# Kernel tuning notes

Measured on AMD Instinct MI355X. Metric: run time of the kernel, lower is better.

Reference implementation:

```python
import jax, jax.numpy as jnp
import numpy as np

N_NODES = 100000
N_EDGES = 1600000
F_IN = 128
N_GRAPHS = 1000
NUM_CLASSES = 2


def setup_inputs() -> dict:
    key = jax.random.key(0)
    ks = jax.random.split(key, 12)
    x = jax.random.normal(ks[0], (N_NODES, F_IN), jnp.float32)
    edge_index = jax.random.randint(ks[1], (2, N_EDGES), 0, N_NODES, dtype=jnp.int32)
    edge_weight = jnp.ones((N_EDGES,), jnp.float32)
    node_graph_index = jnp.sort(
        jax.random.randint(ks[2], (N_NODES,), 0, N_GRAPHS, dtype=jnp.int32))
    s = 0.05
    params = {
        'W0': jax.random.normal(ks[3], (F_IN, 64), jnp.float32) * s,
        'b0': jnp.zeros((64,), jnp.float32),
        'W1': jax.random.normal(ks[4], (64, 32), jnp.float32) * s,
        'b1': jnp.zeros((32,), jnp.float32),
        'Wm1': jax.random.normal(ks[5], (32, 128), jnp.float32) * s,
        'bm1': jnp.zeros((128,), jnp.float32),
        'Wm2': jax.random.normal(ks[6], (128, NUM_CLASSES), jnp.float32) * s,
        'bm2': jnp.zeros((NUM_CLASSES,), jnp.float32),
    }
    return dict(x=x, edge_index=edge_index, edge_weight=edge_weight,
                node_graph_index=node_graph_index, **params)


def _gcn_norm(edge_index, edge_weight, n_nodes):
    # renormalization trick: add self-loops, D^-1/2 (A+I) D^-1/2
    loop = jnp.arange(n_nodes, dtype=edge_index.dtype)
    src = jnp.concatenate([edge_index[0], loop])
    dst = jnp.concatenate([edge_index[1], loop])
    w = jnp.concatenate([edge_weight, jnp.ones((n_nodes,), edge_weight.dtype)])
    deg = jax.ops.segment_sum(w, dst, num_segments=n_nodes)
    dinv = jnp.where(deg > 0, jax.lax.rsqrt(jnp.maximum(deg, 1e-12)), 0.0)
    norm_w = dinv[src] * w * dinv[dst]
    return src, dst, norm_w


def _gcn_layer(h, src, dst, norm_w, W, b, n_nodes):
    m = h @ W                                # [N, out] dense transform first
    msg = m[src] * norm_w[:, None]           # [E+N, out] irregular gather
    agg = jax.ops.segment_sum(msg, dst, num_segments=n_nodes)
    return jax.nn.relu(agg + b)


def reference(x, edge_index, edge_weight, node_graph_index,
              W0, b0, W1, b1, Wm1, bm1, Wm2, bm2):
    n_nodes = x.shape[0]
    src, dst, norm_w = _gcn_norm(edge_index, edge_weight, n_nodes)
    h = _gcn_layer(x, src, dst, norm_w, W0, b0, n_nodes)   # GCN 64 + relu
    # dropout is identity at inference (training=False default)
    h = _gcn_layer(h, src, dst, norm_w, W1, b1, n_nodes)   # GCN 32 + relu
    g = jax.ops.segment_sum(h, node_graph_index, num_segments=N_GRAPHS)  # sum_pool
    g = jax.nn.relu(g @ Wm1 + bm1)
    logits = g @ Wm2 + bm2
    return logits
```

## Files before the change

### kernel.cpp

```cpp
#include <hip/hip_runtime.h>
#include <hip/hip_bf16.h>

#define F_IN 128
#define NPB 256
#define NPB_SH 8
#define MAXB 512
#define CHUNK 4096
#define CAP 5120

typedef __attribute__((ext_vector_type(8))) short short8;
typedef __attribute__((ext_vector_type(4))) float f32x4;


__device__ __forceinline__ float bf2f(unsigned short u) {
    return __uint_as_float(((unsigned int)u) << 16);
}
__device__ __forceinline__ unsigned short f2bf(float f) {
    unsigned int x = __float_as_uint(f);
    x += 0x7FFFu + ((x >> 16) & 1u);
    return (unsigned short)(x >> 16);
}
__device__ __forceinline__ void bf8_fma(float w, uint4 r, float* a) {
    a[0] = fmaf(w, __uint_as_float(r.x << 16), a[0]);
    a[1] = fmaf(w, __uint_as_float(r.x & 0xFFFF0000u), a[1]);
    a[2] = fmaf(w, __uint_as_float(r.y << 16), a[2]);
    a[3] = fmaf(w, __uint_as_float(r.y & 0xFFFF0000u), a[3]);
    a[4] = fmaf(w, __uint_as_float(r.z << 16), a[4]);
    a[5] = fmaf(w, __uint_as_float(r.z & 0xFFFF0000u), a[5]);
    a[6] = fmaf(w, __uint_as_float(r.w << 16), a[6]);
    a[7] = fmaf(w, __uint_as_float(r.w & 0xFFFF0000u), a[7]);
}

__global__ __launch_bounds__(256) void prep_w_kernel(
    const float* __restrict__ W0, const float* __restrict__ W1,
    unsigned short* __restrict__ W0t, unsigned short* __restrict__ W1t,
    int* __restrict__ gcursor, float* __restrict__ Gbuf,
    int nbucket, int gtot) {
    int t = blockIdx.x * 256 + threadIdx.x;
    int stride = gridDim.x * 256;
    for (int o = t; o < 64 * 128; o += stride) {
        int n = o >> 7, k = o & 127;
        W0t[o] = f2bf(W0[k * 64 + n]);
    }
    for (int o = t; o < 32 * 64; o += stride) {
        int n = o >> 6, k = o & 63;
        W1t[o] = f2bf(W1[k * 32 + n]);
    }
    for (int o = t; o < nbucket; o += stride) gcursor[o] = 0;
    for (int o = t; o < gtot; o += stride) Gbuf[o] = 0.f;
}

__global__ __launch_bounds__(1024) void bucket_fused_kernel(
    const int* __restrict__ src, const int* __restrict__ dst,
    const float* __restrict__ ew, int* __restrict__ gcursor,
    int2* __restrict__ tmp, int E, int nbucket) {
    __shared__ int hist[MAXB];
    __shared__ int gbase[MAXB];
    const int tid = threadIdx.x;
    const int e0 = blockIdx.x * CHUNK;
    const int e1 = min(e0 + CHUNK, E);
    for (int b = tid; b < nbucket; b += 1024) hist[b] = 0;
    __syncthreads();
    const int e = e0 + (tid << 2);
    const bool vec = (e + 4 <= e1);
    const int nsc = vec ? 0 : max(0, e1 - e);
    int4 d4 = make_int4(0, 0, 0, 0);
    if (vec) {
        d4 = *(const int4*)(dst + e);
        atomicAdd(&hist[d4.x >> NPB_SH], 1);
        atomicAdd(&hist[d4.y >> NPB_SH], 1);
        atomicAdd(&hist[d4.z >> NPB_SH], 1);
        atomicAdd(&hist[d4.w >> NPB_SH], 1);
    } else {
        for (int j = 0; j < nsc; ++j) {
            int d = dst[e + j];
            ((int*)&d4)[j] = d;
            atomicAdd(&hist[d >> NPB_SH], 1);
        }
    }
    __syncthreads();
    for (int b = tid; b < nbucket; b += 1024) {
        int h = hist[b];
        gbase[b] = (h > 0) ? atomicAdd(&gcursor[b], h) : 0;
        hist[b] = 0;
    }
    __syncthreads();
    if (vec) {
        int4 s4 = *(const int4*)(src + e);
        float4 w4 = *(const float4*)(ew + e);
        {
            int d = d4.x, b = d >> NPB_SH;
            int r = atomicAdd(&hist[b], 1);
            tmp[(size_t)b * CAP + gbase[b] + r] =
                make_int2(s4.x | ((d & (NPB - 1)) << 17), __float_as_int(w4.x));
        }
        {
            int d = d4.y, b = d >> NPB_SH;
            int r = atomicAdd(&hist[b], 1);
            tmp[(size_t)b * CAP + gbase[b] + r] =
                make_int2(s4.y | ((d & (NPB - 1)) << 17), __float_as_int(w4.y));
        }
        {
            int d = d4.z, b = d >> NPB_SH;
            int r = atomicAdd(&hist[b], 1);
            tmp[(size_t)b * CAP + gbase[b] + r] =
                make_int2(s4.z | ((d & (NPB - 1)) << 17), __float_as_int(w4.z));
        }
        {
            int d = d4.w, b = d >> NPB_SH;
            int r = atomicAdd(&hist[b], 1);
            tmp[(size_t)b * CAP + gbase[b] + r] =
                make_int2(s4.w | ((d & (NPB - 1)) << 17), __float_as_int(w4.w));
        }
    } else {
        for (int j = 0; j < nsc; ++j) {
            int d = ((int*)&d4)[j];
            int b = d >> NPB_SH;
            int r = atomicAdd(&hist[b], 1);
            tmp[(size_t)b * CAP + gbase[b] + r] =
                make_int2(src[e + j] | ((d & (NPB - 1)) << 17), __float_as_int(ew[e + j]));
        }
    }
}

__global__ __launch_bounds__(1024) void csr_kernel(
    const int2* __restrict__ tmp, const int* __restrict__ gcursor,
    int2* __restrict__ es, int* __restrict__ rstart, int* __restrict__ rend,
    float* __restrict__ dinv, int N) {
    __shared__ int cnt[256];
    __shared__ float dw[256];
    __shared__ int off[256];
    __shared__ int cur[256];
    const int t = threadIdx.x;
    const int n0 = blockIdx.x << NPB_SH;
    const size_t seg = (size_t)blockIdx.x * CAP;
    if (t < 256) {
        cnt[t] = 0;
        dw[t] = 0.f;
    }
    __syncthreads();
    const int count = gcursor[blockIdx.x];
    const int pairs = count >> 1;
    for (int i = t; i < pairs; i += 1024) {
        int4 v = *(const int4*)(tmp + seg + 2 * i);
        int d0 = v.x >> 17, d1 = v.z >> 17;
        atomicAdd(&cnt[d0], 1);
        atomicAdd(&dw[d0], __int_as_float(v.y));
        atomicAdd(&cnt[d1], 1);
        atomicAdd(&dw[d1], __int_as_float(v.w));
    }
    if ((count & 1) && t == 0) {
        int2 e2 = tmp[seg + count - 1];
        int d = e2.x >> 17;
        atomicAdd(&cnt[d], 1);
        atomicAdd(&dw[d], __int_as_float(e2.y));
    }
    __syncthreads();
    if (t < 256) off[t] = cnt[t];
    __syncthreads();
    for (int o = 1; o < 256; o <<= 1) {
        int x = 0;
        if (t >= o && t < 256) x = off[t - o];
        __syncthreads();
        if (t < 256) off[t] += x;
        __syncthreads();
    }
    if (t < 256) {
        int v = cnt[t];
        int excl = off[t] - v;
        cur[t] = excl;
        int n = n0 + t;
        if (n < N) {
            rstart[n] = (int)seg + excl;
            rend[n] = (int)seg + excl + v;
            dinv[n] = rsqrtf(fmaxf(1.f + dw[t], 1e-12f));
        }
    }
    __syncthreads();
    for (int i = t; i < pairs; i += 1024) {
        int4 v = *(const int4*)(tmp + seg + 2 * i);
        int d0 = v.x >> 17, d1 = v.z >> 17;
        int r0 = atomicAdd(&cur[d0], 1);
        es[seg + r0] = make_int2(v.x & 0x1FFFF, v.y);
        int r1 = atomicAdd(&cur[d1], 1);
        es[seg + r1] = make_int2(v.z & 0x1FFFF, v.w);
    }
    if ((count & 1) && t == 0) {
        int2 e2 = tmp[seg + count - 1];
        int d = e2.x >> 17;
        int r = atomicAdd(&cur[d], 1);
        es[seg + r] = make_int2(e2.x & 0x1FFFF, e2.y);
    }
}

__global__ __launch_bounds__(256) void gemm1_mfma_kernel(
    const float* __restrict__ X, const unsigned short* __restrict__ W0t,
    const float* __restrict__ dinv, unsigned short* __restrict__ M, int N) {
    __shared__ unsigned short Bs[64][136];
    const int tid = threadIdx.x;
    for (int i = tid; i < 64 * 32; i += 256) {
        int n = i >> 5, k4 = i & 31;
        ushort4 v = ((const ushort4*)W0t)[i];
        *(ushort4*)&Bs[n][k4 * 4] = v;
    }
    __syncthreads();
    const int wave = tid >> 6, lane = tid & 63;
    const int m = lane & 15, q = lane >> 4;
    const int rowA = blockIdx.x * 64 + wave * 16 + m;
    const bool rok = rowA < N;
    const float* xrow = X + (size_t)rowA * 128;
    f32x4 acc[4] = {};
#pragma unroll
    for (int ks = 0; ks < 4; ++ks) {
        int k0 = ks * 32 + q * 8;
        float4 u0 = make_float4(0.f, 0.f, 0.f, 0.f);
        float4 u1 = make_float4(0.f, 0.f, 0.f, 0.f);
        if (rok) {
            u0 = *(const float4*)(xrow + k0);
            u1 = *(const float4*)(xrow + k0 + 4);
        }
        short8 a;
        a[0] = (short)f2bf(u0.x); a[1] = (short)f2bf(u0.y);
        a[2] = (short)f2bf(u0.z); a[3] = (short)f2bf(u0.w);
        a[4] = (short)f2bf(u1.x); a[5] = (short)f2bf(u1.y);
        a[6] = (short)f2bf(u1.z); a[7] = (short)f2bf(u1.w);
#pragma unroll
        for (int ct = 0; ct < 4; ++ct) {
            short8 b = *(const short8*)&Bs[ct * 16 + m][k0];
            acc[ct] = __builtin_amdgcn_mfma_f32_16x16x32_bf16(a, b, acc[ct], 0, 0, 0);
        }
    }
#pragma unroll
    for (int r = 0; r < 4; ++r) {
        int crow = blockIdx.x * 64 + wave * 16 + q * 4 + r;
        if (crow < N) {
            float d = dinv[crow];
#pragma unroll
            for (int ct = 0; ct < 4; ++ct)
                M[(size_t)crow * 64 + ct * 16 + m] = f2bf(acc[ct][r] * d);
        }
    }
}

__global__ __launch_bounds__(256) void gemm2_mfma_kernel(
    const unsigned short* __restrict__ H1, const unsigned short* __restrict__ W1t,
    const float* __restrict__ dinv, unsigned short* __restrict__ M, int N) {
    __shared__ unsigned short Bs[32][72];
    const int tid = threadIdx.x;
    for (int i = tid; i < 32 * 16; i += 256) {
        int n = i >> 4, k4 = i & 15;
        ushort4 v = ((const ushort4*)W1t)[i];
        *(ushort4*)&Bs[n][k4 * 4] = v;
    }
    __syncthreads();
    const int wave = tid >> 6, lane = tid & 63;
    const int m = lane & 15, q = lane >> 4;
    const int rowA = blockIdx.x * 64 + wave * 16 + m;
    const bool rok = rowA < N;
    const short8 az = {0, 0, 0, 0, 0, 0, 0, 0};
    f32x4 acc[2] = {};
#pragma unroll
    for (int ks = 0; ks < 2; ++ks) {
        int k0 = ks * 32 + q * 8;
        short8 a = rok ? *(const short8*)(H1 + (size_t)rowA * 64 + k0) : az;
#pragma unroll
        for (int ct = 0; ct < 2; ++ct) {
            short8 b = *(const short8*)&Bs[ct * 16 + m][k0];
            acc[ct] = __builtin_amdgcn_mfma_f32_16x16x32_bf16(a, b, acc[ct], 0, 0, 0);
        }
    }
#pragma unroll
    for (int r = 0; r < 4; ++r) {
        int crow = blockIdx.x * 64 + wave * 16 + q * 4 + r;
        if (crow < N) {
            float d = dinv[crow];
#pragma unroll
            for (int ct = 0; ct < 2; ++ct)
                M[(size_t)crow * 32 + ct * 16 + m] = f2bf(acc[ct][r] * d);
        }
    }
}

__global__ __launch_bounds__(256) void pull1_kernel(
    const int* __restrict__ rstart, const int* __restrict__ rend,
    const int2* __restrict__ es, const unsigned short* __restrict__ M,
    const float* __restrict__ dinv, const float* __restrict__ bias,
    unsigned short* __restrict__ H1, int N) {
    const int lane = threadIdx.x & 63;
    const int wave = threadIdx.x >> 6;
    const int nd = lane >> 5;
    const int node = blockIdx.x * 8 + wave * 2 + nd;
    if (node >= N) return;
    const int c = lane & 7;
    const int q = (lane >> 3) & 3;
    float acc[8] = {0.f, 0.f, 0.f, 0.f, 0.f, 0.f, 0.f, 0.f};
    if (q == 0) {
        uint4 r = *(const uint4*)(M + (size_t)node * 64 + c * 8);
        bf8_fma(1.f, r, acc);
    }
    const int b = rstart[node], e = rend[node];
    const int len = e - b;
    const int base = len >> 2, rem = len & 3;
    int p = b + q * base + min(q, rem);
    const int pe = p + base + (q < rem ? 1 : 0);
    for (; p + 2 <= pe; p += 2) {
        int4 v = *(const int4*)(es + p);
        uint4 r0 = *(const uint4*)(M + (size_t)v.x * 64 + c * 8);
        uint4 r1 = *(const uint4*)(M + (size_t)v.z * 64 + c * 8);
        bf8_fma(__int_as_float(v.y), r0, acc);
        bf8_fma(__int_as_float(v.w), r1, acc);
    }
    if (p < pe) {
        int2 ed = es[p];
        uint4 r = *(const uint4*)(M + (size_t)ed.x * 64 + c * 8);
        bf8_fma(__int_as_float(ed.y), r, acc);
    }
#pragma unroll
    for (int off = 8; off <= 16; off <<= 1)
#pragma unroll
        for (int k = 0; k < 8; ++k) acc[k] += __shfl_xor(acc[k], off);
    if (q == 0) {
        float d = dinv[node];
        const float* bp = bias + c * 8;
        float4 b0v = *(const float4*)(bp);
        float4 b1v = *(const float4*)(bp + 4);
        unsigned short o[8];
        o[0] = f2bf(fmaxf(fmaf(d, acc[0], b0v.x), 0.f));
        o[1] = f2bf(fmaxf(fmaf(d, acc[1], b0v.y), 0.f));
        o[2] = f2bf(fmaxf(fmaf(d, acc[2], b0v.z), 0.f));
        o[3] = f2bf(fmaxf(fmaf(d, acc[3], b0v.w), 0.f));
        o[4] = f2bf(fmaxf(fmaf(d, acc[4], b1v.x), 0.f));
        o[5] = f2bf(fmaxf(fmaf(d, acc[5], b1v.y), 0.f));
        o[6] = f2bf(fmaxf(fmaf(d, acc[6], b1v.z), 0.f));
        o[7] = f2bf(fmaxf(fmaf(d, acc[7], b1v.w), 0.f));
        uint4 pk;
        pk.x = (unsigned int)o[0] | ((unsigned int)o[1] << 16);
        pk.y = (unsigned int)o[2] | ((unsigned int)o[3] << 16);
        pk.z = (unsigned int)o[4] | ((unsigned int)o[5] << 16);
        pk.w = (unsigned int)o[6] | ((unsigned int)o[7] << 16);
        *(uint4*)(H1 + (size_t)node * 64 + c * 8) = pk;
    }
}

__global__ __launch_bounds__(256) void pull2_pool_kernel(
    const int* __restrict__ rstart, const int* __restrict__ rend,
    const int2* __restrict__ es, const unsigned short* __restrict__ M,
    const float* __restrict__ dinv, const float* __restrict__ bias,
    const int* __restrict__ ngi, float* __restrict__ g, int N) {
    __shared__ float4 sh[16][8];
    __shared__ int sgx[16];
    const int t = threadIdx.x;
    const int lane = t & 63;
    const int nl = t >> 4;
    const int node = blockIdx.x * 16 + nl;
    const int c = lane & 3;
    const int q = (lane >> 2) & 3;
    const bool valid = node < N;
    float acc[8] = {0.f, 0.f, 0.f, 0.f, 0.f, 0.f, 0.f, 0.f};
    if (valid) {
        if (q == 0) {
            uint4 r = *(const uint4*)(M + (size_t)node * 32 + c * 8);
            bf8_fma(1.f, r, acc);
        }
        const int b = rstart[node], e = rend[node];
        const int len = e - b;
        const int base = len >> 2, rem = len & 3;
        int p = b + q * base + min(q, rem);
        const int pe = p + base + (q < rem ? 1 : 0);
        for (; p + 2 <= pe; p += 2) {
            int4 v = *(const int4*)(es + p);
            uint4 r0 = *(const uint4*)(M + (size_t)v.x * 32 + c * 8);
            uint4 r1 = *(const uint4*)(M + (size_t)v.z * 32 + c * 8);
            bf8_fma(__int_as_float(v.y), r0, acc);
            bf8_fma(__int_as_float(v.w), r1, acc);
        }
        if (p < pe) {
            int2 ed = es[p];
            uint4 r = *(const uint4*)(M + (size_t)ed.x * 32 + c * 8);
            bf8_fma(__int_as_float(ed.y), r, acc);
        }
#pragma unroll
        for (int off = 4; off <= 8; off <<= 1)
#pragma unroll
            for (int k = 0; k < 8; ++k) acc[k] += __shfl_xor(acc[k], off);
    }
    if (q == 0) {
        float4 o0 = make_float4(0.f, 0.f, 0.f, 0.f);
        float4 o1 = make_float4(0.f, 0.f, 0.f, 0.f);
        if (valid) {
            float d = dinv[node];
            const float* bp = bias + c * 8;
            float4 b0v = *(const float4*)(bp);
            float4 b1v = *(const float4*)(bp + 4);
            o0.x = fmaxf(fmaf(d, acc[0], b0v.x), 0.f);
            o0.y = fmaxf(fmaf(d, acc[1], b0v.y), 0.f);
            o0.z = fmaxf(fmaf(d, acc[2], b0v.z), 0.f);
            o0.w = fmaxf(fmaf(d, acc[3], b0v.w), 0.f);
            o1.x = fmaxf(fmaf(d, acc[4], b1v.x), 0.f);
            o1.y = fmaxf(fmaf(d, acc[5], b1v.y), 0.f);
            o1.z = fmaxf(fmaf(d, acc[6], b1v.z), 0.f);
            o1.w = fmaxf(fmaf(d, acc[7], b1v.w), 0.f);
        }
        sh[nl][c * 2] = o0;
        sh[nl][c * 2 + 1] = o1;
        if (c == 0) sgx[nl] = valid ? ngi[node] : -1;
    }
    __syncthreads();
    if (t < 8) {
        int cc = t;
        float4 a = make_float4(0.f, 0.f, 0.f, 0.f);
        int cg = -1;
        for (int i = 0; i < 16; ++i) {
            int gi = sgx[i];
            if (gi < 0) continue;
            if (gi != cg) {
                if (cg >= 0) {
                    float* gp = g + cg * 32 + cc * 4;
                    atomicAdd(gp + 0, a.x); atomicAdd(gp + 1, a.y);
                    atomicAdd(gp + 2, a.z); atomicAdd(gp + 3, a.w);
                }
                cg = gi;
                a = sh[i][cc];
            } else {
                float4 tv = sh[i][cc];
                a.x += tv.x; a.y += tv.y; a.z += tv.z; a.w += tv.w;
            }
        }
        if (cg >= 0) {
            float* gp = g + cg * 32 + cc * 4;
            atomicAdd(gp + 0, a.x); atomicAdd(gp + 1, a.y);
            atomicAdd(gp + 2, a.z); atomicAdd(gp + 3, a.w);
        }
    }
}

__global__ __launch_bounds__(128) void mlp_kernel(
    const float* __restrict__ g, const float* __restrict__ Wm1,
    const float* __restrict__ bm1, const float* __restrict__ Wm2,
    const float* __restrict__ bm2, float* __restrict__ out) {
    __shared__ float sg[32];
    __shared__ float red[4];
    int b = blockIdx.x, t = threadIdx.x;
    if (t < 32) sg[t] = g[b * 32 + t];
    __syncthreads();
    float acc = bm1[t];
#pragma unroll
    for (int k = 0; k < 32; ++k) acc = fmaf(sg[k], Wm1[k * 128 + t], acc);
    float h = fmaxf(acc, 0.f);
    float p0 = h * Wm2[t * 2 + 0];
    float p1 = h * Wm2[t * 2 + 1];
#pragma unroll
    for (int off = 32; off >= 1; off >>= 1) {
        p0 += __shfl_xor(p0, off);
        p1 += __shfl_xor(p1, off);
    }
    if ((t & 63) == 0) {
        red[(t >> 6) * 2 + 0] = p0;
        red[(t >> 6) * 2 + 1] = p1;
    }
    __syncthreads();
    if (t < 2) out[b * 2 + t] = bm2[t] + red[t] + red[2 + t];
}


extern "C" void kernel_launch(void* const* d_in, const int* in_sizes, int n_in,
                              void* d_out, int out_size, void* d_ws, size_t ws_size,
                              hipStream_t stream) {
    const float* x   = (const float*)d_in[0];
    const int*   ei  = (const int*)d_in[1];
    const float* ew  = (const float*)d_in[2];
    const int*   ngi = (const int*)d_in[3];
    const float* W0  = (const float*)d_in[4];
    const float* b0  = (const float*)d_in[5];
    const float* W1  = (const float*)d_in[6];
    const float* b1  = (const float*)d_in[7];
    const float* Wm1 = (const float*)d_in[8];
    const float* bm1 = (const float*)d_in[9];
    const float* Wm2 = (const float*)d_in[10];
    const float* bm2 = (const float*)d_in[11];
    float* out = (float*)d_out;

    const int N = in_sizes[0] / F_IN;
    const int E = in_sizes[1] / 2;
    const int G = out_size / 2;
    const int* srcp = ei;
    const int* dstp = ei + E;
    const int NBUCKET = (N + NPB - 1) >> NPB_SH;
    const int NBLK = (E + CHUNK - 1) / CHUNK;

    char* wsb = (char*)d_ws;
    size_t off = 0;
    auto alloc = [&](size_t bytes) {
        char* p = wsb + off;
        off += (bytes + 255) & ~(size_t)255;
        return p;
    };
    float* dinv     = (float*)alloc((size_t)N * 4);
    int*   gcursor  = (int*)  alloc((size_t)NBUCKET * 4);
    int*   rstart   = (int*)  alloc((size_t)N * 4);
    int*   rend     = (int*)  alloc((size_t)N * 4);
    int2*  tmp      = (int2*) alloc((size_t)NBUCKET * CAP * 8);
    int2*  es       = (int2*) alloc((size_t)NBUCKET * CAP * 8);
    unsigned short* W0t = (unsigned short*)alloc(64 * 128 * 2);
    unsigned short* W1t = (unsigned short*)alloc(32 * 64 * 2);
    unsigned short* M   = (unsigned short*)alloc((size_t)N * 64 * 2);
    unsigned short* H1  = (unsigned short*)alloc((size_t)N * 64 * 2);
    float* Gbuf     = (float*)alloc((size_t)G * 32 * 4);
    unsigned short* m1p = M;

    prep_w_kernel<<<8, 256, 0, stream>>>(W0, W1, W0t, W1t, gcursor, Gbuf, NBUCKET, G * 32);
    bucket_fused_kernel<<<NBLK, 1024, 0, stream>>>(srcp, dstp, ew, gcursor, tmp, E, NBUCKET);
    csr_kernel<<<NBUCKET, 1024, 0, stream>>>(tmp, gcursor, es, rstart, rend, dinv, N);

    gemm1_mfma_kernel<<<(N + 63) / 64, 256, 0, stream>>>(x, W0t, dinv, M, N);
    pull1_kernel<<<(N + 7) / 8, 256, 0, stream>>>(rstart, rend, es, M, dinv, b0, H1, N);

    gemm2_mfma_kernel<<<(N + 63) / 64, 256, 0, stream>>>(H1, W1t, dinv, m1p, N);
    pull2_pool_kernel<<<(N + 15) / 16, 256, 0, stream>>>(rstart, rend, es, m1p, dinv, b1, ngi, Gbuf, N);

    mlp_kernel<<<G, 128, 0, stream>>>(Gbuf, Wm1, bm1, Wm2, bm2, out);
}
```

Before: 240.2 us.

## Drop shared float atomics for degree, unroll gathers by four, use unsafe atomics

The CSR build no longer accumulates edge weights with float atomics in shared memory. Instead, each node's degree is summed serially from its already-sorted edge segment after the scatter. Both aggregation kernels unroll the edge gather loop to four edges per iteration so more independent row loads are in flight. Graph pooling switches to unsafeAtomicAdd so the hardware float atomic can be used. The serial per-thread degree sum adds a strided read pass and could create imbalance when a node has many edges.

```diff
diff --git a/kernel.cpp b/kernel.cpp
--- a/kernel.cpp
+++ b/kernel.cpp
@@ -29,6 +29,9 @@
     a[5] = fmaf(w, __uint_as_float(r.z & 0xFFFF0000u), a[5]);
     a[6] = fmaf(w, __uint_as_float(r.w << 16), a[6]);
     a[7] = fmaf(w, __uint_as_float(r.w & 0xFFFF0000u), a[7]);
+}
+__device__ __forceinline__ void fadd_global(float* p, float v) {
+    unsafeAtomicAdd(p, v);
 }
 
 __global__ __launch_bounds__(256) void prep_w_kernel(
@@ -128,35 +131,30 @@
     int2* __restrict__ es, int* __restrict__ rstart, int* __restrict__ rend,
     float* __restrict__ dinv, int N) {
     __shared__ int cnt[256];
-    __shared__ float dw[256];
     __shared__ int off[256];
     __shared__ int cur[256];
     const int t = threadIdx.x;
     const int n0 = blockIdx.x << NPB_SH;
     const size_t seg = (size_t)blockIdx.x * CAP;
-    if (t < 256) {
-        cnt[t] = 0;
-        dw[t] = 0.f;
-    }
+    if (t < 256) cnt[t] = 0;
     __syncthreads();
     const int count = gcursor[blockIdx.x];
     const int pairs = count >> 1;
     for (int i = t; i < pairs; i += 1024) {
         int4 v = *(const int4*)(tmp + seg + 2 * i);
-        int d0 = v.x >> 17, d1 = v.z >> 17;
-        atomicAdd(&cnt[d0], 1);
-        atomicAdd(&dw[d0], __int_as_float(v.y));
-        atomicAdd(&cnt[d1], 1);
-        atomicAdd(&dw[d1], __int_as_float(v.w));
+        atomicAdd(&cnt[v.x >> 17], 1);
+        atomicAdd(&cnt[v.z >> 17], 1);
     }
     if ((count & 1) && t == 0) {
         int2 e2 = tmp[seg + count - 1];
-        int d = e2.x >> 17;
-        atomicAdd(&cnt[d], 1);
-        atomicAdd(&dw[d], __int_as_float(e2.y));
-    }
-    __syncthreads();
-    if (t < 256) off[t] = cnt[t];
+        atomicAdd(&cnt[e2.x >> 17], 1);
+    }
+    __syncthreads();
+    int myc = 0, excl = 0;
+    if (t < 256) {
+        myc = cnt[t];
+        off[t] = myc;
+    }
     __syncthreads();
     for (int o = 1; o < 256; o <<= 1) {
         int x = 0;
@@ -166,14 +164,12 @@
         __syncthreads();
     }
     if (t < 256) {
-        int v = cnt[t];
-        int excl = off[t] - v;
+        excl = off[t] - myc;
         cur[t] = excl;
         int n = n0 + t;
         if (n < N) {
             rstart[n] = (int)seg + excl;
-            rend[n] = (int)seg + excl + v;
-            dinv[n] = rsqrtf(fmaxf(1.f + dw[t], 1e-12f));
+            rend[n] = (int)seg + excl + myc;
         }
     }
     __syncthreads();
@@ -190,6 +186,16 @@
         int d = e2.x >> 17;
         int r = atomicAdd(&cur[d], 1);
         es[seg + r] = make_int2(e2.x & 0x1FFFF, e2.y);
+    }
+    __syncthreads();
+    if (t < 256) {
+        int n = n0 + t;
+        if (n < N) {
+            float s = 0.f;
+            const int2* ep = es + seg + excl;
+            for (int j = 0; j < myc; ++j) s += __int_as_float(ep[j].y);
+            dinv[n] = rsqrtf(fmaxf(1.f + s, 1e-12f));
+        }
     }
 }
 
@@ -303,12 +309,25 @@
     const int base = len >> 2, rem = len & 3;
     int p = b + q * base + min(q, rem);
     const int pe = p + base + (q < rem ? 1 : 0);
-    for (; p + 2 <= pe; p += 2) {
+    for (; p + 4 <= pe; p += 4) {
+        int4 v0 = *(const int4*)(es + p);
+        int4 v1 = *(const int4*)(es + p + 2);
+        uint4 r0 = *(const uint4*)(M + (size_t)v0.x * 64 + c * 8);
+        uint4 r1 = *(const uint4*)(M + (size_t)v0.z * 64 + c * 8);
+        uint4 r2 = *(const uint4*)(M + (size_t)v1.x * 64 + c * 8);
+        uint4 r3 = *(const uint4*)(M + (size_t)v1.z * 64 + c * 8);
+        bf8_fma(__int_as_float(v0.y), r0, acc);
+        bf8_fma(__int_as_float(v0.w), r1, acc);
+        bf8_fma(__int_as_float(v1.y), r2, acc);
+        bf8_fma(__int_as_float(v1.w), r3, acc);
+    }
+    if (p + 2 <= pe) {
         int4 v = *(const int4*)(es + p);
         uint4 r0 = *(const uint4*)(M + (size_t)v.x * 64 + c * 8);
         uint4 r1 = *(const uint4*)(M + (size_t)v.z * 64 + c * 8);
         bf8_fma(__int_as_float(v.y), r0, acc);
         bf8_fma(__int_as_float(v.w), r1, acc);
+        p += 2;
     }
     if (p < pe) {
         int2 ed = es[p];
@@ -367,12 +386,25 @@
         const int base = len >> 2, rem = len & 3;
         int p = b + q * base + min(q, rem);
         const int pe = p + base + (q < rem ? 1 : 0);
-        for (; p + 2 <= pe; p += 2) {
+        for (; p + 4 <= pe; p += 4) {
+            int4 v0 = *(const int4*)(es + p);
+            int4 v1 = *(const int4*)(es + p + 2);
+            uint4 r0 = *(const uint4*)(M + (size_t)v0.x * 32 + c * 8);
+            uint4 r1 = *(const uint4*)(M + (size_t)v0.z * 32 + c * 8);
+            uint4 r2 = *(const uint4*)(M + (size_t)v1.x * 32 + c * 8);
+            uint4 r3 = *(const uint4*)(M + (size_t)v1.z * 32 + c * 8);
+            bf8_fma(__int_as_float(v0.y), r0, acc);
+            bf8_fma(__int_as_float(v0.w), r1, acc);
+            bf8_fma(__int_as_float(v1.y), r2, acc);
+            bf8_fma(__int_as_float(v1.w), r3, acc);
+        }
+        if (p + 2 <= pe) {
             int4 v = *(const int4*)(es + p);
             uint4 r0 = *(const uint4*)(M + (size_t)v.x * 32 + c * 8);
             uint4 r1 = *(const uint4*)(M + (size_t)v.z * 32 + c * 8);
             bf8_fma(__int_as_float(v.y), r0, acc);
             bf8_fma(__int_as_float(v.w), r1, acc);
+            p += 2;
         }
         if (p < pe) {
             int2 ed = es[p];
@@ -416,8 +448,8 @@
             if (gi != cg) {
                 if (cg >= 0) {
                     float* gp = g + cg * 32 + cc * 4;
-                    atomicAdd(gp + 0, a.x); atomicAdd(gp + 1, a.y);
-                    atomicAdd(gp + 2, a.z); atomicAdd(gp + 3, a.w);
+                    fadd_global(gp + 0, a.x); fadd_global(gp + 1, a.y);
+                    fadd_global(gp + 2, a.z); fadd_global(gp + 3, a.w);
                 }
                 cg = gi;
                 a = sh[i][cc];
@@ -428,8 +460,8 @@
         }
         if (cg >= 0) {
             float* gp = g + cg * 32 + cc * 4;
-            atomicAdd(gp + 0, a.x); atomicAdd(gp + 1, a.y);
-            atomicAdd(gp + 2, a.z); atomicAdd(gp + 3, a.w);
+            fadd_global(gp + 0, a.x); fadd_global(gp + 1, a.y);
+            fadd_global(gp + 2, a.z); fadd_global(gp + 3, a.w);
         }
     }
 }
```

Measured after the change: 250.9 us. 1.04x slower.
